# Kernel tuning notes

Hardware: AMD Instinct MI355X
Metric: run time of the kernel (lower is better)

## Reference

```python
import jax, jax.numpy as jnp
import numpy as np

D_MODEL = 1024
NUM_HEADS = 16
HEAD_DIM = D_MODEL // NUM_HEADS


def setup_inputs() -> dict:
    key = jax.random.key(0)
    ks = jax.random.split(key, 11)
    B, S = 2, 2048
    scale = 1.0 / np.sqrt(D_MODEL)
    inp = {
        "q": jax.random.normal(ks[0], (B, S, D_MODEL), jnp.float32),
        "k": jax.random.normal(ks[1], (B, S, D_MODEL), jnp.float32),
        "v": jax.random.normal(ks[2], (B, S, D_MODEL), jnp.float32),
        "Wq": jax.random.normal(ks[3], (D_MODEL, D_MODEL), jnp.float32) * scale,
        "bq": jnp.zeros((D_MODEL,), jnp.float32),
        "Wk": jax.random.normal(ks[4], (D_MODEL, D_MODEL), jnp.float32) * scale,
        "bk": jnp.zeros((D_MODEL,), jnp.float32),
        "Wv": jax.random.normal(ks[5], (D_MODEL, D_MODEL), jnp.float32) * scale,
        "bv": jnp.zeros((D_MODEL,), jnp.float32),
        "Wo": jax.random.normal(ks[6], (D_MODEL, D_MODEL), jnp.float32) * scale,
        "bo": jnp.zeros((D_MODEL,), jnp.float32),
    }
    return inp


def reference(q, k, v, Wq, bq, Wk, bk, Wv, bv, Wo, bo):
    B, S, _ = q.shape
    # Linear projections (torch Linear: x @ W.T + b), split into heads -> [b,h,s,d]
    def proj(x, W, b):
        y = jnp.einsum('bsm,nm->bsn', x, W) + b
        return y.reshape(B, -1, NUM_HEADS, HEAD_DIM).transpose(0, 2, 1, 3)
    qh = proj(q, Wq, bq)
    kh = proj(k, Wk, bk)
    vh = proj(v, Wv, bv)
    # NOTE: source scales by sqrt(d_model), NOT sqrt(head_dim) -- faithful quirk
    factor = jnp.sqrt(jnp.float32(D_MODEL))
    scores = jnp.einsum('bhqd,bhkd->bhqk', qh, kh) / factor
    attn = jax.nn.softmax(scores, axis=-1)
    out = jnp.einsum('bhqk,bhkd->bhqd', attn, vh)
    out = out.transpose(0, 2, 1, 3).reshape(B, S, D_MODEL)
    # out projection; dropout=0.0 (eval) is identity
    return jnp.einsum('bsm,nm->bsn', out, Wo) + bo
```

## Files before the change

### kernel.cpp

```cpp
#include <hip/hip_runtime.h>
#include <hip/hip_bf16.h>

typedef __hip_bfloat16 bf16;
typedef short short8 __attribute__((ext_vector_type(8)));
typedef short bs4 __attribute__((ext_vector_type(4)));
typedef float f32x4 __attribute__((ext_vector_type(4)));
typedef float f32x16 __attribute__((ext_vector_type(16)));

#define MFMA_BF16(a, b, c) __builtin_amdgcn_mfma_f32_16x16x32_bf16(a, b, c, 0, 0, 0)
#define MFMA32_BF16(a, b, c) __builtin_amdgcn_mfma_f32_32x32x16_bf16(a, b, c, 0, 0, 0)

#define QSCALE 0.045084439f

__device__ __forceinline__ void async_copy16(const bf16* g, bf16* l) {
    __builtin_amdgcn_global_load_lds(
        (const __attribute__((address_space(1))) unsigned int*)(const void*)g,
        (__attribute__((address_space(3))) unsigned int*)(void*)l, 16, 0, 0);
}

__global__ __launch_bounds__(256) void convert_all(
    const float* __restrict__ q, const float* __restrict__ k, const float* __restrict__ v,
    const float* __restrict__ wq, const float* __restrict__ wk,
    const float* __restrict__ wv, const float* __restrict__ wo,
    bf16* __restrict__ qb, bf16* __restrict__ kb, bf16* __restrict__ vb,
    bf16* __restrict__ wqb, bf16* __restrict__ wkb, bf16* __restrict__ wvb,
    bf16* __restrict__ wob)
{
    int blk = blockIdx.x;
    const float* s; bf16* d; int rel;
    if      (blk < 1024) { s = q;  d = qb;  rel = blk; }
    else if (blk < 2048) { s = k;  d = kb;  rel = blk - 1024; }
    else if (blk < 3072) { s = v;  d = vb;  rel = blk - 2048; }
    else if (blk < 3328) { s = wq; d = wqb; rel = blk - 3072; }
    else if (blk < 3584) { s = wk; d = wkb; rel = blk - 3328; }
    else if (blk < 3840) { s = wv; d = wvb; rel = blk - 3584; }
    else                 { s = wo; d = wob; rel = blk - 3840; }
    size_t base = (size_t)rel * 1024 + threadIdx.x;
#pragma unroll
    for (int i = 0; i < 4; i++) {
        float4 f = ((const float4*)s)[base + i * 256];
        union { bf16 h[4]; uint2 u; } pk;
        pk.h[0] = (bf16)f.x; pk.h[1] = (bf16)f.y;
        pk.h[2] = (bf16)f.z; pk.h[3] = (bf16)f.w;
        ((uint2*)d)[base + i * 256] = pk.u;
    }
}

__global__ __launch_bounds__(256) void gemm_qkv(
    const bf16* __restrict__ qb, const bf16* __restrict__ kb, const bf16* __restrict__ vb,
    const bf16* __restrict__ wqb, const bf16* __restrict__ wkb, const bf16* __restrict__ wvb,
    const float* __restrict__ bq, const float* __restrict__ bk, const float* __restrict__ bv,
    bf16* __restrict__ Qp, bf16* __restrict__ Kp, bf16* __restrict__ Vt)
{
    __shared__ bf16 Al[128 * 64];
    __shared__ bf16 Bl[128 * 64];

    const int sel = blockIdx.y >> 3;
    const bf16* A; const bf16* W; const float* bias;
    if      (sel == 0) { A = qb; W = wqb; bias = bq; }
    else if (sel == 1) { A = kb; W = wkb; bias = bk; }
    else               { A = vb; W = wvb; bias = bv; }

    const int K = 1024, N = 1024;
    const int t = threadIdx.x;
    const int lane = t & 63, wave = t >> 6;
    const int ln = lane & 15, quad = lane >> 4;
    const int wm = wave >> 1, wn = wave & 1;
    const int m0 = blockIdx.x * 128, n0 = (blockIdx.y & 7) * 128;

    f32x4 acc[4][4];
#pragma unroll
    for (int i = 0; i < 4; i++)
#pragma unroll
        for (int j = 0; j < 4; j++) acc[i][j] = (f32x4){0.f, 0.f, 0.f, 0.f};

    const int lk = ln & 7;
    const int srow = t >> 3, sidx0 = t & 7;

    for (int k0 = 0; k0 < K; k0 += 64) {
        const bf16* Ab = A + (size_t)m0 * K + k0;
        const bf16* Wb = W + (size_t)n0 * K + k0;
#pragma unroll
        for (int p = 0; p < 4; p++) {
            int row = p * 32 + srow, idx = sidx0 ^ (row & 7);
            async_copy16(Ab + (size_t)row * K + idx * 8, &Al[(p * 256 + wave * 64) * 8]);
        }
#pragma unroll
        for (int p = 0; p < 4; p++) {
            int row = p * 32 + srow, idx = sidx0 ^ (row & 7);
            async_copy16(Wb + (size_t)row * K + idx * 8, &Bl[(p * 256 + wave * 64) * 8]);
        }
        __syncthreads();

#pragma unroll
        for (int kk = 0; kk < 2; kk++) {
            short8 af[4], bfr[4];
#pragma unroll
            for (int i = 0; i < 4; i++) {
                int r = wm * 64 + i * 16 + ln;
                af[i] = *(const short8*)&Al[r * 64 + (((kk << 2) | quad) ^ lk) * 8];
            }
#pragma unroll
            for (int j = 0; j < 4; j++) {
                int r = wn * 64 + j * 16 + ln;
                bfr[j] = *(const short8*)&Bl[r * 64 + (((kk << 2) | quad) ^ lk) * 8];
            }
#pragma unroll
            for (int i = 0; i < 4; i++)
#pragma unroll
                for (int j = 0; j < 4; j++)
                    acc[i][j] = MFMA_BF16(af[i], bfr[j], acc[i][j]);
        }
        __syncthreads();
    }

#pragma unroll
    for (int j = 0; j < 4; j++) {
        int c = n0 + wn * 64 + j * 16 + ln;
        float bv2 = bias[c];
        if (sel == 2) {
            int h = c >> 6, dd = c & 63;
#pragma unroll
            for (int i = 0; i < 4; i++) {
                int m = m0 + wm * 64 + i * 16 + quad * 4;
                int bb = m >> 11, s = m & 2047;
                union { bf16 h4[4]; uint2 u; } pk;
#pragma unroll
                for (int r = 0; r < 4; r++) pk.h4[r] = (bf16)(acc[i][j][r] + bv2);
                *(uint2*)&Vt[(((size_t)(bb * 16 + h)) * 64 + dd) * 2048 + s] = pk.u;
            }
        } else {
            bf16* out = (sel == 0) ? Qp : Kp;
            float scl = (sel == 0) ? QSCALE : 1.0f;
#pragma unroll
            for (int i = 0; i < 4; i++) {
                int rb = m0 + wm * 64 + i * 16 + quad * 4;
#pragma unroll
                for (int r = 0; r < 4; r++)
                    out[(size_t)(rb + r) * N + c] = (bf16)((acc[i][j][r] + bv2) * scl);
            }
        }
    }
}

__global__ __launch_bounds__(256) void gemm_fin(
    const bf16* __restrict__ A, const bf16* __restrict__ W,
    const float* __restrict__ bias, float* __restrict__ C)
{
    __shared__ bf16 Al[2][128 * 64];
    __shared__ bf16 Bl[2][128 * 64];

    const int K = 1024, N = 1024;
    const int t = threadIdx.x;
    const int lane = t & 63, wave = t >> 6;
    const int ln = lane & 15, quad = lane >> 4;
    const int wm = wave >> 1, wn = wave & 1;
    const int m0 = blockIdx.x * 128, n0 = blockIdx.y * 128;

    f32x4 acc[4][4];
#pragma unroll
    for (int i = 0; i < 4; i++)
#pragma unroll
        for (int j = 0; j < 4; j++) acc[i][j] = (f32x4){0.f, 0.f, 0.f, 0.f};

    const int lk = ln & 7;
    const int srow = t >> 3, sidx0 = t & 7;

#define STAGE_AB(buf_, k0_) do {                                               \
    const bf16* Ab = A + (size_t)m0 * K + (k0_);                               \
    const bf16* Wb = W + (size_t)n0 * K + (k0_);                               \
    _Pragma("unroll")                                                          \
    for (int p = 0; p < 4; p++) {                                              \
        int row = p * 32 + srow, idx = sidx0 ^ (row & 7);                      \
        async_copy16(Ab + (size_t)row * K + idx * 8,                           \
                     &Al[buf_][(p * 256 + wave * 64) * 8]);                    \
    }                                                                          \
    _Pragma("unroll")                                                          \
    for (int p = 0; p < 4; p++) {                                              \
        int row = p * 32 + srow, idx = sidx0 ^ (row & 7);                      \
        async_copy16(Wb + (size_t)row * K + idx * 8,                           \
                     &Bl[buf_][(p * 256 + wave * 64) * 8]);                    \
    }                                                                          \
} while (0)

    STAGE_AB(0, 0);

    for (int k0 = 0; k0 < K; k0 += 64) {
        const int cur = (k0 >> 6) & 1;
        if (k0 < K - 64) {
            STAGE_AB(cur ^ 1, k0 + 64);
            asm volatile("s_waitcnt vmcnt(8)" ::: "memory");
        } else {
            asm volatile("s_waitcnt vmcnt(0)" ::: "memory");
        }
        __builtin_amdgcn_s_barrier();

        const bf16* Alc = Al[cur];
        const bf16* Blc = Bl[cur];

#pragma unroll
        for (int kk = 0; kk < 2; kk++) {
            short8 af[4], bfr[4];
#pragma unroll
            for (int i = 0; i < 4; i++) {
                int r = wm * 64 + i * 16 + ln;
                af[i] = *(const short8*)&Alc[r * 64 + (((kk << 2) | quad) ^ lk) * 8];
            }
#pragma unroll
            for (int j = 0; j < 4; j++) {
                int r = wn * 64 + j * 16 + ln;
                bfr[j] = *(const short8*)&Blc[r * 64 + (((kk << 2) | quad) ^ lk) * 8];
            }
            __builtin_amdgcn_s_setprio(1);
#pragma unroll
            for (int i = 0; i < 4; i++)
#pragma unroll
                for (int j = 0; j < 4; j++)
                    acc[i][j] = MFMA_BF16(af[i], bfr[j], acc[i][j]);
            __builtin_amdgcn_s_setprio(0);
        }

        asm volatile("" ::: "memory");
        __builtin_amdgcn_s_barrier();
    }
#undef STAGE_AB

#pragma unroll
    for (int j = 0; j < 4; j++) {
        int c = n0 + wn * 64 + j * 16 + ln;
        float bv2 = bias[c];
#pragma unroll
        for (int i = 0; i < 4; i++) {
            int rb = m0 + wm * 64 + i * 16 + quad * 4;
#pragma unroll
            for (int r = 0; r < 4; r++)
                C[(size_t)(rb + r) * N + c] = acc[i][j][r] + bv2;
        }
    }
}

__global__ __launch_bounds__(512, 4) void attn128q(
    const bf16* __restrict__ Q, const bf16* __restrict__ K,
    const bf16* __restrict__ V, bf16* __restrict__ O)
{
    const int S = 2048, D = 1024;
    __shared__ bf16 Kl[2][128 * 64];
    __shared__ bf16 Vl[2][64 * 128];

    const int t = threadIdx.x, lane = t & 63, wave = t >> 6;
    const int lo = lane & 31, hi = lane >> 5;
    const int keyhalf = wave >> 2;
    const int qw = wave & 3;
    const int h = blockIdx.x & 15, b = blockIdx.x >> 4, qt = blockIdx.y;
    const size_t kqbase = (size_t)b * S * D + (size_t)h * 64;
    const size_t vbase = ((size_t)(b * 16 + h)) * 64 * 2048;

    const int q0 = qt * 128 + qw * 32;
    short8 aq[4];
    {
        const bf16* qp = Q + kqbase + (size_t)(q0 + lo) * D + hi * 8;
#pragma unroll
        for (int s = 0; s < 4; s++) aq[s] = *(const short8*)(qp + s * 16);
    }
    asm volatile("" :: "v"(aq[0]), "v"(aq[1]), "v"(aq[2]), "v"(aq[3]));

    f32x16 o0, o1;
#pragma unroll
    for (int i = 0; i < 16; i++) { o0[i] = 0.f; o1[i] = 0.f; }
    f32x4 l4 = (f32x4){0.f, 0.f, 0.f, 0.f};

    int koff[4];
#pragma unroll
    for (int s = 0; s < 4; s++)
        koff[s] = lo * 64 + (((2 * s + hi) ^ (lo & 7)) * 8);
    const int khbase = keyhalf * 64 * 64;

    const int x0 = (keyhalf * 8) ^ (lo & 15);
    const int vbl = lo * 128 + hi * 4;

    const int krow = t >> 3, kidx = t & 7;
    const int vrow = t >> 4, vidx = t & 15;

#define STAGE_KV(buf_, kt_) do {                                               \
    _Pragma("unroll")                                                          \
    for (int p = 0; p < 2; p++) {                                              \
        int row = p * 64 + krow, idx = kidx ^ (row & 7);                       \
        async_copy16(K + kqbase + (size_t)((kt_) * 128 + row) * D + idx * 8,   \
                     &Kl[buf_][(p * 512 + wave * 64) * 8]);                    \
    }                                                                          \
    _Pragma("unroll")                                                          \
    for (int p = 0; p < 2; p++) {                                              \
        int row = p * 32 + vrow, idx = vidx ^ (row & 15);                      \
        async_copy16(V + vbase + (size_t)row * 2048 + (kt_) * 128 + idx * 8,   \
                     &Vl[buf_][(p * 512 + wave * 64) * 8]);                    \
    }                                                                          \
} while (0)

    STAGE_KV(0, 0);

    for (int kt = 0; kt < S / 128; kt++) {
        const int cur = kt & 1;
        if (kt < S / 128 - 1) {
            STAGE_KV(cur ^ 1, kt + 1);
            asm volatile("s_waitcnt vmcnt(4)" ::: "memory");
        } else {
            asm volatile("s_waitcnt vmcnt(0)" ::: "memory");
        }
        __builtin_amdgcn_s_barrier();

        const bf16* Klc = Kl[cur];
        const bf16* Vlc = Vl[cur];

#pragma unroll
        for (int kg = 0; kg < 2; kg++) {
            const bf16* kb = Klc + khbase + kg * (32 * 64);
            short8 kf0 = *(const short8*)(kb + koff[0]);
            short8 kf1 = *(const short8*)(kb + koff[1]);
            short8 kf2 = *(const short8*)(kb + koff[2]);
            short8 kf3 = *(const short8*)(kb + koff[3]);

            __builtin_amdgcn_s_setprio(1);
            f32x16 acc;
#pragma unroll
            for (int i = 0; i < 16; i++) acc[i] = 0.f;
            acc = MFMA32_BF16(kf0, aq[0], acc);
            acc = MFMA32_BF16(kf1, aq[1], acc);
            acc = MFMA32_BF16(kf2, aq[2], acc);
            acc = MFMA32_BF16(kf3, aq[3], acc);
            __builtin_amdgcn_s_setprio(0);

            union { bf16 hh[8]; short8 s; } pk0, pk1;
#pragma unroll
            for (int r = 0; r < 8; r++) {
                float p = __builtin_amdgcn_exp2f(acc[r]);
                l4[r & 3] += p;
                pk0.hh[r] = (bf16)p;
            }
#pragma unroll
            for (int r = 0; r < 8; r++) {
                float p = __builtin_amdgcn_exp2f(acc[8 + r]);
                l4[r & 3] += p;
                pk1.hh[r] = (bf16)p;
            }

            __builtin_amdgcn_s_setprio(1);
#pragma unroll
            for (int db = 0; db < 2; db++) {
#pragma unroll
                for (int c = 0; c < 2; c++) {
                    const int m = kg * 4 + 2 * c;
                    union { bs4 hh[2]; short8 s; } vf;
                    vf.hh[0] = *(const bs4*)&Vlc[vbl + db * 4096 + ((x0 ^ m) * 8)];
                    vf.hh[1] = *(const bs4*)&Vlc[vbl + db * 4096 + ((x0 ^ (m + 1)) * 8)];
                    if (db == 0) o0 = MFMA32_BF16(c ? pk1.s : pk0.s, vf.s, o0);
                    else         o1 = MFMA32_BF16(c ? pk1.s : pk0.s, vf.s, o1);
                }
            }
            __builtin_amdgcn_s_setprio(0);
        }

        asm volatile("" ::: "memory");
        __builtin_amdgcn_s_barrier();
    }
#undef STAGE_KV

    float lv = (l4[0] + l4[1]) + (l4[2] + l4[3]);
    lv += __shfl_xor(lv, 32);

    float* os = (float*)&Kl[0][0];
    float* ls = (float*)&Vl[0][0];
    if (wave >= 4) {
        const int w4 = wave - 4;
#pragma unroll
        for (int i = 0; i < 16; i++) os[(w4 * 32 + i) * 64 + lane] = o0[i];
#pragma unroll
        for (int i = 0; i < 16; i++) os[(w4 * 32 + 16 + i) * 64 + lane] = o1[i];
        ls[w4 * 64 + lane] = lv;
    }
    __syncthreads();
    if (wave < 4) {
#pragma unroll
        for (int i = 0; i < 16; i++) o0[i] += os[(wave * 32 + i) * 64 + lane];
#pragma unroll
        for (int i = 0; i < 16; i++) o1[i] += os[(wave * 32 + 16 + i) * 64 + lane];
        lv += ls[wave * 64 + lane];
        float inv = __builtin_amdgcn_rcpf(lv);
#pragma unroll
        for (int r = 0; r < 16; r++) {
            const int q = (r & 3) + 8 * (r >> 2) + 4 * hi;
            float invr = __shfl(inv, q);
            const int row = qt * 128 + qw * 32 + q;
            bf16* op = O + ((size_t)b * S + row) * D + h * 64 + lo;
            op[0]  = (bf16)(o0[r] * invr);
            op[32] = (bf16)(o1[r] * invr);
        }
    }
}

extern "C" void kernel_launch(void* const* d_in, const int* in_sizes, int n_in,
                              void* d_out, int out_size, void* d_ws, size_t ws_size,
                              hipStream_t stream) {
    (void)in_sizes; (void)n_in; (void)out_size; (void)ws_size;
    const float* q  = (const float*)d_in[0];
    const float* k  = (const float*)d_in[1];
    const float* v  = (const float*)d_in[2];
    const float* Wq = (const float*)d_in[3];
    const float* bq = (const float*)d_in[4];
    const float* Wk = (const float*)d_in[5];
    const float* bk = (const float*)d_in[6];
    const float* Wv = (const float*)d_in[7];
    const float* bv = (const float*)d_in[8];
    const float* Wo = (const float*)d_in[9];
    const float* bo = (const float*)d_in[10];
    float* out = (float*)d_out;

    const int M = 4096, N = 1024;
    const size_t MN = (size_t)M * N;
    const size_t NN = (size_t)N * N;
    bf16* qb  = (bf16*)d_ws;
    bf16* kb  = qb + MN;
    bf16* vb  = kb + MN;
    bf16* wqb = vb + MN;
    bf16* wkb = wqb + NN;
    bf16* wvb = wkb + NN;
    bf16* wob = wvb + NN;
    bf16* Qp  = wob + NN;
    bf16* Kp  = Qp + MN;
    bf16* Vt  = Kp + MN;
    bf16* AO  = qb;

    dim3 blk(256);
    convert_all<<<4096, blk, 0, stream>>>(q, k, v, Wq, Wk, Wv, Wo,
                                          qb, kb, vb, wqb, wkb, wvb, wob);

    gemm_qkv<<<dim3(32, 24), blk, 0, stream>>>(qb, kb, vb, wqb, wkb, wvb,
                                               bq, bk, bv, Qp, Kp, Vt);

    attn128q<<<dim3(32, 16), dim3(512), 0, stream>>>(Qp, Kp, Vt, AO);

    gemm_fin<<<dim3(32, 8), blk, 0, stream>>>(AO, wob, bo, out);
}
```

Measured before the change: 223.5 us.

## Split attention key tiles across four wave groups with 1024-thread blocks

The attention block grows from 512 to 1024 threads, so each 128-key tile is split four ways across wave groups (32 keys each) instead of two ways of 64. Each wave does half the per-tile MFMA work and each thread issues one K and one V async copy. The partial outputs and row sums are merged by a two-stage shared-memory tree reduction. The aim is more waves in flight to hide latency, at the cost of an extra reduction stage, more barriers and higher register/LDS pressure per block.

```diff
diff --git a/kernel.cpp b/kernel.cpp
--- a/kernel.cpp
+++ b/kernel.cpp
@@ -239,17 +239,18 @@
     }
 }
 
-__global__ __launch_bounds__(512, 4) void attn128q(
+__global__ __launch_bounds__(1024, 8) void attn128q(
     const bf16* __restrict__ Q, const bf16* __restrict__ K,
     const bf16* __restrict__ V, bf16* __restrict__ O)
 {
     const int S = 2048, D = 1024;
     __shared__ bf16 Kl[2][128 * 64];
     __shared__ bf16 Vl[2][64 * 128];
+    __shared__ float lsc[16 * 64];
 
     const int t = threadIdx.x, lane = t & 63, wave = t >> 6;
     const int lo = lane & 31, hi = lane >> 5;
-    const int keyhalf = wave >> 2;
+    const int kq = wave >> 2;
     const int qw = wave & 3;
     const int h = blockIdx.x & 15, b = blockIdx.x >> 4, qt = blockIdx.y;
     const size_t kqbase = (size_t)b * S * D + (size_t)h * 64;
@@ -269,31 +270,20 @@
     for (int i = 0; i < 16; i++) { o0[i] = 0.f; o1[i] = 0.f; }
     f32x4 l4 = (f32x4){0.f, 0.f, 0.f, 0.f};
 
-    int koff[4];
-#pragma unroll
-    for (int s = 0; s < 4; s++)
-        koff[s] = lo * 64 + (((2 * s + hi) ^ (lo & 7)) * 8);
-    const int khbase = keyhalf * 64 * 64;
-
-    const int x0 = (keyhalf * 8) ^ (lo & 15);
-    const int vbl = lo * 128 + hi * 4;
-
-    const int krow = t >> 3, kidx = t & 7;
-    const int vrow = t >> 4, vidx = t & 15;
+    const int krowb = (kq * 32 + lo) * 64;
+    const int lk7 = lo & 7, lk15 = lo & 15;
+    const int vrow0 = lo * 128 + 4 * hi;
+
+    const int skrow = t >> 3, skidx = t & 7;
+    const int svrow = t >> 4, svidx = t & 15;
 
 #define STAGE_KV(buf_, kt_) do {                                               \
-    _Pragma("unroll")                                                          \
-    for (int p = 0; p < 2; p++) {                                              \
-        int row = p * 64 + krow, idx = kidx ^ (row & 7);                       \
-        async_copy16(K + kqbase + (size_t)((kt_) * 128 + row) * D + idx * 8,   \
-                     &Kl[buf_][(p * 512 + wave * 64) * 8]);                    \
-    }                                                                          \
-    _Pragma("unroll")                                                          \
-    for (int p = 0; p < 2; p++) {                                              \
-        int row = p * 32 + vrow, idx = vidx ^ (row & 15);                      \
-        async_copy16(V + vbase + (size_t)row * 2048 + (kt_) * 128 + idx * 8,   \
-                     &Vl[buf_][(p * 512 + wave * 64) * 8]);                    \
-    }                                                                          \
+    { int row = skrow, idx = skidx ^ (row & 7);                                \
+      async_copy16(K + kqbase + (size_t)((kt_) * 128 + row) * D + idx * 8,     \
+                   &Kl[buf_][wave * 512]); }                                   \
+    { int row = svrow, idx = svidx ^ (row & 15);                               \
+      async_copy16(V + vbase + (size_t)row * 2048 + (kt_) * 128 + idx * 8,     \
+                   &Vl[buf_][wave * 512]); }                                   \
 } while (0)
 
     STAGE_KV(0, 0);
@@ -302,7 +292,7 @@
         const int cur = kt & 1;
         if (kt < S / 128 - 1) {
             STAGE_KV(cur ^ 1, kt + 1);
-            asm volatile("s_waitcnt vmcnt(4)" ::: "memory");
+            asm volatile("s_waitcnt vmcnt(2)" ::: "memory");
         } else {
             asm volatile("s_waitcnt vmcnt(0)" ::: "memory");
         }
@@ -311,53 +301,52 @@
         const bf16* Klc = Kl[cur];
         const bf16* Vlc = Vl[cur];
 
-#pragma unroll
-        for (int kg = 0; kg < 2; kg++) {
-            const bf16* kb = Klc + khbase + kg * (32 * 64);
-            short8 kf0 = *(const short8*)(kb + koff[0]);
-            short8 kf1 = *(const short8*)(kb + koff[1]);
-            short8 kf2 = *(const short8*)(kb + koff[2]);
-            short8 kf3 = *(const short8*)(kb + koff[3]);
-
-            __builtin_amdgcn_s_setprio(1);
-            f32x16 acc;
-#pragma unroll
-            for (int i = 0; i < 16; i++) acc[i] = 0.f;
-            acc = MFMA32_BF16(kf0, aq[0], acc);
-            acc = MFMA32_BF16(kf1, aq[1], acc);
-            acc = MFMA32_BF16(kf2, aq[2], acc);
-            acc = MFMA32_BF16(kf3, aq[3], acc);
-            __builtin_amdgcn_s_setprio(0);
-
-            union { bf16 hh[8]; short8 s; } pk0, pk1;
-#pragma unroll
-            for (int r = 0; r < 8; r++) {
-                float p = __builtin_amdgcn_exp2f(acc[r]);
-                l4[r & 3] += p;
-                pk0.hh[r] = (bf16)p;
-            }
-#pragma unroll
-            for (int r = 0; r < 8; r++) {
-                float p = __builtin_amdgcn_exp2f(acc[8 + r]);
-                l4[r & 3] += p;
-                pk1.hh[r] = (bf16)p;
-            }
-
-            __builtin_amdgcn_s_setprio(1);
-#pragma unroll
-            for (int db = 0; db < 2; db++) {
-#pragma unroll
-                for (int c = 0; c < 2; c++) {
-                    const int m = kg * 4 + 2 * c;
-                    union { bs4 hh[2]; short8 s; } vf;
-                    vf.hh[0] = *(const bs4*)&Vlc[vbl + db * 4096 + ((x0 ^ m) * 8)];
-                    vf.hh[1] = *(const bs4*)&Vlc[vbl + db * 4096 + ((x0 ^ (m + 1)) * 8)];
-                    if (db == 0) o0 = MFMA32_BF16(c ? pk1.s : pk0.s, vf.s, o0);
-                    else         o1 = MFMA32_BF16(c ? pk1.s : pk0.s, vf.s, o1);
-                }
-            }
-            __builtin_amdgcn_s_setprio(0);
-        }
+        short8 kf0 = *(const short8*)&Klc[krowb + (((0 | hi) ^ lk7) * 8)];
+        short8 kf1 = *(const short8*)&Klc[krowb + (((2 | hi) ^ lk7) * 8)];
+        short8 kf2 = *(const short8*)&Klc[krowb + (((4 | hi) ^ lk7) * 8)];
+        short8 kf3 = *(const short8*)&Klc[krowb + (((6 | hi) ^ lk7) * 8)];
+
+        __builtin_amdgcn_s_setprio(1);
+        f32x16 acc;
+#pragma unroll
+        for (int i = 0; i < 16; i++) acc[i] = 0.f;
+        acc = MFMA32_BF16(kf0, aq[0], acc);
+        acc = MFMA32_BF16(kf1, aq[1], acc);
+        acc = MFMA32_BF16(kf2, aq[2], acc);
+        acc = MFMA32_BF16(kf3, aq[3], acc);
+        __builtin_amdgcn_s_setprio(0);
+
+        union { bf16 hh[8]; short8 s; } pk0, pk1;
+#pragma unroll
+        for (int r = 0; r < 8; r++) {
+            float p = __builtin_amdgcn_exp2f(acc[r]);
+            l4[r & 3] += p;
+            pk0.hh[r] = (bf16)p;
+        }
+#pragma unroll
+        for (int r = 0; r < 8; r++) {
+            float p = __builtin_amdgcn_exp2f(acc[8 + r]);
+            l4[r & 3] += p;
+            pk1.hh[r] = (bf16)p;
+        }
+
+        __builtin_amdgcn_s_setprio(1);
+        {
+            union { bs4 h2[2]; short8 s; } vf;
+            vf.h2[0] = *(const bs4*)&Vlc[vrow0 + (((kq * 4 + 0) ^ lk15) * 8)];
+            vf.h2[1] = *(const bs4*)&Vlc[vrow0 + (((kq * 4 + 1) ^ lk15) * 8)];
+            o0 = MFMA32_BF16(pk0.s, vf.s, o0);
+            vf.h2[0] = *(const bs4*)&Vlc[vrow0 + (((kq * 4 + 2) ^ lk15) * 8)];
+            vf.h2[1] = *(const bs4*)&Vlc[vrow0 + (((kq * 4 + 3) ^ lk15) * 8)];
+            o0 = MFMA32_BF16(pk1.s, vf.s, o0);
+            vf.h2[0] = *(const bs4*)&Vlc[vrow0 + 4096 + (((kq * 4 + 0) ^ lk15) * 8)];
+            vf.h2[1] = *(const bs4*)&Vlc[vrow0 + 4096 + (((kq * 4 + 1) ^ lk15) * 8)];
+            o1 = MFMA32_BF16(pk0.s, vf.s, o1);
+            vf.h2[0] = *(const bs4*)&Vlc[vrow0 + 4096 + (((kq * 4 + 2) ^ lk15) * 8)];
+            vf.h2[1] = *(const bs4*)&Vlc[vrow0 + 4096 + (((kq * 4 + 3) ^ lk15) * 8)];
+            o1 = MFMA32_BF16(pk1.s, vf.s, o1);
+        }
+        __builtin_amdgcn_s_setprio(0);
 
         asm volatile("" ::: "memory");
         __builtin_amdgcn_s_barrier();
@@ -366,30 +355,48 @@
 
     float lv = (l4[0] + l4[1]) + (l4[2] + l4[3]);
     lv += __shfl_xor(lv, 32);
-
-    float* os = (float*)&Kl[0][0];
-    float* ls = (float*)&Vl[0][0];
-    if (wave >= 4) {
-        const int w4 = wave - 4;
-#pragma unroll
-        for (int i = 0; i < 16; i++) os[(w4 * 32 + i) * 64 + lane] = o0[i];
-#pragma unroll
-        for (int i = 0; i < 16; i++) os[(w4 * 32 + 16 + i) * 64 + lane] = o1[i];
-        ls[w4 * 64 + lane] = lv;
+    lsc[wave * 64 + lane] = lv;
+
+    float* sK = (float*)&Kl[0][0];
+    float* sV = (float*)&Vl[0][0];
+    if (kq >= 2) {
+        float* sp = (kq == 2) ? (sK + qw * 2048) : (sV + qw * 2048);
+#pragma unroll
+        for (int i = 0; i < 16; i++) sp[i * 64 + lane] = o0[i];
+#pragma unroll
+        for (int i = 0; i < 16; i++) sp[(16 + i) * 64 + lane] = o1[i];
     }
     __syncthreads();
-    if (wave < 4) {
-#pragma unroll
-        for (int i = 0; i < 16; i++) o0[i] += os[(wave * 32 + i) * 64 + lane];
-#pragma unroll
-        for (int i = 0; i < 16; i++) o1[i] += os[(wave * 32 + 16 + i) * 64 + lane];
-        lv += ls[wave * 64 + lane];
-        float inv = __builtin_amdgcn_rcpf(lv);
+    if (kq < 2) {
+        const float* sp = (kq == 0) ? (sK + qw * 2048) : (sV + qw * 2048);
+#pragma unroll
+        for (int i = 0; i < 16; i++) o0[i] += sp[i * 64 + lane];
+#pragma unroll
+        for (int i = 0; i < 16; i++) o1[i] += sp[(16 + i) * 64 + lane];
+    }
+    __syncthreads();
+    if (kq == 1) {
+        float* sp = sK + qw * 2048;
+#pragma unroll
+        for (int i = 0; i < 16; i++) sp[i * 64 + lane] = o0[i];
+#pragma unroll
+        for (int i = 0; i < 16; i++) sp[(16 + i) * 64 + lane] = o1[i];
+    }
+    __syncthreads();
+    if (kq == 0) {
+        const float* sp = sK + qw * 2048;
+#pragma unroll
+        for (int i = 0; i < 16; i++) o0[i] += sp[i * 64 + lane];
+#pragma unroll
+        for (int i = 0; i < 16; i++) o1[i] += sp[(16 + i) * 64 + lane];
+        float lt = lsc[(0 * 4 + qw) * 64 + lane] + lsc[(1 * 4 + qw) * 64 + lane]
+                 + lsc[(2 * 4 + qw) * 64 + lane] + lsc[(3 * 4 + qw) * 64 + lane];
+        float inv = __builtin_amdgcn_rcpf(lt);
 #pragma unroll
         for (int r = 0; r < 16; r++) {
-            const int q = (r & 3) + 8 * (r >> 2) + 4 * hi;
-            float invr = __shfl(inv, q);
-            const int row = qt * 128 + qw * 32 + q;
+            const int qrel = (r & 3) + 8 * (r >> 2) + 4 * hi;
+            float invr = __shfl(inv, qrel);
+            const int row = q0 + qrel;
             bf16* op = O + ((size_t)b * S + row) * D + h * 64 + lo;
             op[0]  = (bf16)(o0[r] * invr);
             op[32] = (bf16)(o1[r] * invr);
@@ -436,7 +443,7 @@
     gemm_qkv<<<dim3(32, 24), blk, 0, stream>>>(qb, kb, vb, wqb, wkb, wvb,
                                                bq, bk, bv, Qp, Kp, Vt);
 
-    attn128q<<<dim3(32, 16), dim3(512), 0, stream>>>(Qp, Kp, Vt, AO);
+    attn128q<<<dim3(32, 16), dim3(1024), 0, stream>>>(Qp, Kp, Vt, AO);
 
     gemm_fin<<<dim3(32, 8), blk, 0, stream>>>(AO, wob, bo, out);
 }
```

After: 516.1 us. 131% more time.
